# Kernel optimization log

Hardware: AMD Instinct MI355X
Metric: run time of the kernel (lower is better)

## Reference

```python
import jax, jax.numpy as jnp
import numpy as np

N_HEADS = 16
D_HEAD = 64
QUERY_DIM = 1024
CONTEXT_DIM = 1024
INNER = N_HEADS * D_HEAD


def setup_inputs() -> dict:
    key = jax.random.key(0)
    ks = jax.random.split(key, 7)
    B, Nq, Nk = 4, 1024, 1024
    x = jax.random.normal(ks[0], (B, Nq, QUERY_DIM), dtype=jnp.float32)
    context = jax.random.normal(ks[1], (B, Nk, CONTEXT_DIM), dtype=jnp.float32)
    s_q = 1.0 / np.sqrt(QUERY_DIM)
    s_c = 1.0 / np.sqrt(CONTEXT_DIM)
    s_i = 1.0 / np.sqrt(INNER)
    Wq = jax.random.uniform(ks[2], (QUERY_DIM, INNER), jnp.float32, -s_q, s_q)
    Wk = jax.random.uniform(ks[3], (CONTEXT_DIM, INNER), jnp.float32, -s_c, s_c)
    Wv = jax.random.uniform(ks[4], (CONTEXT_DIM, INNER), jnp.float32, -s_c, s_c)
    Wo = jax.random.uniform(ks[5], (INNER, QUERY_DIM), jnp.float32, -s_i, s_i)
    bo = jax.random.uniform(ks[6], (QUERY_DIM,), jnp.float32, -s_i, s_i)
    return {"x": x, "context": context, "Wq": Wq, "Wk": Wk, "Wv": Wv, "Wo": Wo, "bo": bo}


def reference(x, context, Wq, Wk, Wv, Wo, bo):
    B, Nq, _ = x.shape
    Nk = context.shape[1]
    scale = D_HEAD ** -0.5
    # project and split heads: [B, H, N, d]
    q = (x @ Wq).reshape(B, Nq, N_HEADS, D_HEAD).transpose(0, 2, 1, 3)
    k = (context @ Wk).reshape(B, Nk, N_HEADS, D_HEAD).transpose(0, 2, 1, 3)
    v = (context @ Wv).reshape(B, Nk, N_HEADS, D_HEAD).transpose(0, 2, 1, 3)
    scores = jnp.einsum("bhqd,bhkd->bhqk", q, k) * scale
    attn = jax.nn.softmax(scores, axis=-1)
    out = jnp.einsum("bhqk,bhkd->bhqd", attn, v)
    out = out.transpose(0, 2, 1, 3).reshape(B, Nq, INNER)
    return out @ Wo + bo
```

## Files before the change

### kernel.cpp

```cpp
#include <hip/hip_runtime.h>
#include <hip/hip_bf16.h>

#define BATCH 4
#define NQ 1024
#define NKK 1024
#define HD 1024
#define NHEADS 16

typedef __bf16 bf16x8 __attribute__((ext_vector_type(8)));
typedef float f32x4 __attribute__((ext_vector_type(4)));
typedef unsigned short u16;
typedef unsigned int u32;

__device__ __forceinline__ u16 f2bf(float f) {
    union { float f; u32 u; } v; v.f = f;
    u32 r = v.u + 0x7FFFu + ((v.u >> 16) & 1u);
    return (u16)(r >> 16);
}

#define GLOAD16(gp, lp) \
    __builtin_amdgcn_global_load_lds((const __attribute__((address_space(1))) void*)(gp), \
                                     (__attribute__((address_space(3))) void*)(lp), 16, 0, 0)

#define MFMA16(a, b, c) __builtin_amdgcn_mfma_f32_16x16x32_bf16(a, b, c, 0, 0, 0)

__global__ __launch_bounds__(256) void cvt2bf_k(const float* __restrict__ a,
                                                u16* __restrict__ o, int n4) {
    int i = blockIdx.x * blockDim.x + threadIdx.x;
    const int stride = gridDim.x * blockDim.x;
    for (; i < n4; i += stride) {
        float4 v = ((const float4*)a)[i];
        ushort4 p;
        p.x = f2bf(v.x); p.y = f2bf(v.y); p.z = f2bf(v.z); p.w = f2bf(v.w);
        ((ushort4*)o)[i] = p;
    }
}

__global__ __launch_bounds__(256) void transpose4_k(const float* __restrict__ w0,
                                                    const float* __restrict__ w1,
                                                    const float* __restrict__ w2,
                                                    const float* __restrict__ w3,
                                                    u16* __restrict__ ws) {
    const float* src = blockIdx.z == 0 ? w0 : blockIdx.z == 1 ? w1 : blockIdx.z == 2 ? w2 : w3;
    const float scl = (blockIdx.z == 0) ? 0.18033688011112042f : 1.0f;
    u16* dst = ws + (size_t)blockIdx.z * (1024u * 1024u);
    __shared__ u16 t[64][65];
    const int bx = blockIdx.x * 64;
    const int by = blockIdx.y * 64;
    const int tid = threadIdx.x;
#pragma unroll
    for (int p = 0; p < 16; ++p) {
        int idx = p * 256 + tid;
        int r = idx >> 6, c = idx & 63;
        t[c][r] = f2bf(scl * src[(size_t)(by + r) * 1024 + bx + c]);
    }
    __syncthreads();
#pragma unroll
    for (int p = 0; p < 16; ++p) {
        int idx = p * 256 + tid;
        int r = idx >> 6, c = idx & 63;
        dst[(size_t)(bx + r) * 1024 + by + c] = t[r][c];
    }
}

__global__ __launch_bounds__(256) void gemm_qkv(const u16* __restrict__ Xb,
                                                const u16* __restrict__ Cb,
                                                const u16* __restrict__ WqT,
                                                const u16* __restrict__ WkT,
                                                const u16* __restrict__ WvT,
                                                u16* __restrict__ Qb,
                                                u16* __restrict__ Kb,
                                                u16* __restrict__ VTb) {
    const int bid = blockIdx.x;
    const int swz = (bid & 7) * 192 + (bid >> 3);
    const int z = swz / 512;
    const int rem = swz - z * 512;
    const int m0 = (rem >> 3) * 64;
    const int n0 = (rem & 7) * 128;

    const u16* __restrict__ A  = (z == 0) ? Xb : Cb;
    const u16* __restrict__ BT = (z == 0) ? WqT : (z == 1) ? WkT : WvT;

    __shared__ __align__(16) u16 Asm[64 * 32];
    __shared__ __align__(16) u16 Bsm[128 * 32];

    const int tid = threadIdx.x, lane = tid & 63, wv = tid >> 6;
    const int wm = wv >> 1, wn = wv & 1;
    const int lr = lane & 15, lg = lane >> 4;
    const int M = BATCH * NQ, N = HD, K = HD;

    const int sa = wv * 64 + lane;
    const int ra = sa >> 2, ka = (sa & 3) * 8;
    const int cb0 = (wv * 2) * 64, cb1 = (wv * 2 + 1) * 64;
    const int s0 = cb0 + lane, s1 = cb1 + lane;
    const int r0 = s0 >> 2, k0 = (s0 & 3) * 8;
    const int r1 = s1 >> 2, k1 = (s1 & 3) * 8;

    f32x4 acc[2][4];
#pragma unroll
    for (int i = 0; i < 2; ++i)
#pragma unroll
        for (int j = 0; j < 4; ++j) acc[i][j] = (f32x4)(0.0f);

    for (int kt = 0; kt < K; kt += 32) {
        __syncthreads();
        GLOAD16(A + (size_t)(m0 + ra) * K + kt + ka, &Asm[(wv * 64) * 8]);
        GLOAD16(BT + (size_t)(n0 + r0) * K + kt + k0, &Bsm[cb0 * 8]);
        GLOAD16(BT + (size_t)(n0 + r1) * K + kt + k1, &Bsm[cb1 * 8]);
        __syncthreads();
        bf16x8 af[2], bfr[4];
#pragma unroll
        for (int m = 0; m < 2; ++m)
            af[m] = *(const bf16x8*)&Asm[(wm * 32 + m * 16 + lr) * 32 + lg * 8];
#pragma unroll
        for (int n = 0; n < 4; ++n)
            bfr[n] = *(const bf16x8*)&Bsm[(wn * 64 + n * 16 + lr) * 32 + lg * 8];
#pragma unroll
        for (int m = 0; m < 2; ++m)
#pragma unroll
            for (int n = 0; n < 4; ++n)
                acc[m][n] = MFMA16(af[m], bfr[n], acc[m][n]);
    }

    if (z < 2) {
        u16* __restrict__ C = (z == 0) ? Qb : Kb;
#pragma unroll
        for (int m = 0; m < 2; ++m)
#pragma unroll
            for (int n = 0; n < 4; ++n) {
                const int col = n0 + wn * 64 + n * 16 + lr;
                const int rb = m0 + wm * 32 + m * 16 + lg * 4;
#pragma unroll
                for (int r = 0; r < 4; ++r)
                    C[(size_t)(rb + r) * N + col] = f2bf(acc[m][n][r]);
            }
    } else {
#pragma unroll
        for (int m = 0; m < 2; ++m)
#pragma unroll
            for (int n = 0; n < 4; ++n) {
                const int col = n0 + wn * 64 + n * 16 + lr;
                const int rb = m0 + wm * 32 + m * 16 + lg * 4;
                ushort4 pk;
                pk.x = f2bf(acc[m][n][0]);
                pk.y = f2bf(acc[m][n][1]);
                pk.z = f2bf(acc[m][n][2]);
                pk.w = f2bf(acc[m][n][3]);
                *(ushort4*)&VTb[(size_t)col * M + rb] = pk;
            }
    }
}

__global__ __launch_bounds__(256) void gemm_out(const u16* __restrict__ A,
                                                const u16* __restrict__ BT,
                                                const float* __restrict__ bias,
                                                float* __restrict__ C) {
    const int bid = blockIdx.x;
    const int swz = (bid & 7) * 64 + (bid >> 3);
    const int m0 = (swz >> 3) * 64;
    const int n0 = (swz & 7) * 128;

    __shared__ __align__(16) u16 Asm[64 * 32];
    __shared__ __align__(16) u16 Bsm[128 * 32];

    const int tid = threadIdx.x, lane = tid & 63, wv = tid >> 6;
    const int wm = wv >> 1, wn = wv & 1;
    const int lr = lane & 15, lg = lane >> 4;
    const int N = HD, K = HD;

    const int sa = wv * 64 + lane;
    const int ra = sa >> 2, ka = (sa & 3) * 8;
    const int cb0 = (wv * 2) * 64, cb1 = (wv * 2 + 1) * 64;
    const int s0 = cb0 + lane, s1 = cb1 + lane;
    const int r0 = s0 >> 2, k0 = (s0 & 3) * 8;
    const int r1 = s1 >> 2, k1 = (s1 & 3) * 8;

    f32x4 acc[2][4];
#pragma unroll
    for (int i = 0; i < 2; ++i)
#pragma unroll
        for (int j = 0; j < 4; ++j) acc[i][j] = (f32x4)(0.0f);

    for (int kt = 0; kt < K; kt += 32) {
        __syncthreads();
        GLOAD16(A + (size_t)(m0 + ra) * K + kt + ka, &Asm[(wv * 64) * 8]);
        GLOAD16(BT + (size_t)(n0 + r0) * K + kt + k0, &Bsm[cb0 * 8]);
        GLOAD16(BT + (size_t)(n0 + r1) * K + kt + k1, &Bsm[cb1 * 8]);
        __syncthreads();
        bf16x8 af[2], bfr[4];
#pragma unroll
        for (int m = 0; m < 2; ++m)
            af[m] = *(const bf16x8*)&Asm[(wm * 32 + m * 16 + lr) * 32 + lg * 8];
#pragma unroll
        for (int n = 0; n < 4; ++n)
            bfr[n] = *(const bf16x8*)&Bsm[(wn * 64 + n * 16 + lr) * 32 + lg * 8];
#pragma unroll
        for (int m = 0; m < 2; ++m)
#pragma unroll
            for (int n = 0; n < 4; ++n)
                acc[m][n] = MFMA16(af[m], bfr[n], acc[m][n]);
    }

#pragma unroll
    for (int m = 0; m < 2; ++m)
#pragma unroll
        for (int n = 0; n < 4; ++n) {
            const int col = n0 + wn * 64 + n * 16 + lr;
            const int rb = m0 + wm * 32 + m * 16 + lg * 4;
            const float bv = bias[col];
#pragma unroll
            for (int r = 0; r < 4; ++r)
                C[(size_t)(rb + r) * N + col] = acc[m][n][r] + bv;
        }
}

__global__ __launch_bounds__(256) void attn_k(const u16* __restrict__ Q,
                                              const u16* __restrict__ Kp,
                                              const u16* __restrict__ VT,
                                              u16* __restrict__ AO) {
    __shared__ __align__(16) u16 Ksm[2][64 * 64];
    __shared__ __align__(16) u16 Vsm[2][64 * 64];
    __shared__ __align__(16) u16 Psm[4][16 * 64];

    const int tid = threadIdx.x, lane = tid & 63, wv = tid >> 6;
    const int lr = lane & 15, lg = lane >> 4;

    const int swz = (blockIdx.x & 7) * 128 + (blockIdx.x >> 3);
    const int bh = swz >> 4;
    const int b = bh >> 4, h = bh & 15;
    const int q0 = (swz & 15) * 64 + wv * 16;
    const int lx = lr & 7;

    bf16x8 qf[2];
#pragma unroll
    for (int ks = 0; ks < 2; ++ks)
        qf[ks] = *(const bf16x8*)&Q[(size_t)(b * NQ + q0 + lr) * HD +
                                    h * 64 + ks * 32 + lg * 8];

    const int kbase = b * NKK, vrow0 = h * 64;
    auto stageKV = [&](int kt, int bufsel) {
#pragma unroll
        for (int i = 0; i < 2; ++i) {
            const int cb = (wv * 2 + i) * 64;
            const int s = cb + lane;
            const int row = s >> 3;
            const int cg = (s & 7) ^ (row & 7);
            GLOAD16(Kp + (size_t)(kbase + kt + row) * HD + h * 64 + cg * 8,
                    &Ksm[bufsel][cb * 8]);
            GLOAD16(VT + (size_t)(vrow0 + row) * (BATCH * NKK) + kbase + kt + cg * 8,
                    &Vsm[bufsel][cb * 8]);
        }
    };

    float sum[4] = {0.0f, 0.0f, 0.0f, 0.0f};
    f32x4 o[4];
#pragma unroll
    for (int n = 0; n < 4; ++n) o[n] = (f32x4)(0.0f);

    stageKV(0, 0);
    __syncthreads();
    int cur = 0;

    for (int t = 0; t < NKK / 64; ++t) {
        if (t + 1 < NKK / 64) stageKV((t + 1) * 64, cur ^ 1);
        const u16* Ks = &Ksm[cur][0];
        const u16* Vs = &Vsm[cur][0];

        f32x4 s[4];
#pragma unroll
        for (int n = 0; n < 4; ++n) s[n] = (f32x4)(0.0f);
#pragma unroll
        for (int n = 0; n < 4; ++n) {
            bf16x8 kf0 = *(const bf16x8*)&Ks[(n * 16 + lr) * 64 + (lg ^ lx) * 8];
            bf16x8 kf1 = *(const bf16x8*)&Ks[(n * 16 + lr) * 64 + ((lg | 4) ^ lx) * 8];
            s[n] = MFMA16(qf[0], kf0, s[n]);
            s[n] = MFMA16(qf[1], kf1, s[n]);
        }

        u16* P = &Psm[wv][0];
#pragma unroll
        for (int n = 0; n < 4; ++n)
#pragma unroll
            for (int r = 0; r < 4; ++r) {
                const float p = exp2f(s[n][r]);
                sum[r] += p;
                const int row = lg * 4 + r;
                const int c = n * 2 + (lr >> 3);
                P[row * 64 + ((c ^ (row & 7)) * 8) + (lr & 7)] = f2bf(p);
            }

#pragma unroll
        for (int ks = 0; ks < 2; ++ks) {
            bf16x8 pa = *(const bf16x8*)&P[lr * 64 + (((ks * 4 + lg) ^ lx)) * 8];
#pragma unroll
            for (int n = 0; n < 4; ++n) {
                bf16x8 vf = *(const bf16x8*)&Vs[(n * 16 + lr) * 64 + (((ks * 4 + lg) ^ lx)) * 8];
                o[n] = MFMA16(pa, vf, o[n]);
            }
        }
        __syncthreads();
        cur ^= 1;
    }

    float rs[4];
#pragma unroll
    for (int r = 0; r < 4; ++r) {
        float v = sum[r];
#pragma unroll
        for (int d = 1; d < 16; d <<= 1) v += __shfl_xor(v, d);
        rs[r] = 1.0f / v;
    }

#pragma unroll
    for (int n = 0; n < 4; ++n)
#pragma unroll
        for (int r = 0; r < 4; ++r) {
            const float v = o[n][r] * rs[r];
            AO[(size_t)(b * NQ + q0 + lg * 4 + r) * HD +
               h * 64 + n * 16 + lr] = f2bf(v);
        }
}

extern "C" void kernel_launch(void* const* d_in, const int* in_sizes, int n_in,
                              void* d_out, int out_size, void* d_ws, size_t ws_size,
                              hipStream_t stream) {
    const float* x   = (const float*)d_in[0];
    const float* ctx = (const float*)d_in[1];
    const float* Wq  = (const float*)d_in[2];
    const float* Wk  = (const float*)d_in[3];
    const float* Wv  = (const float*)d_in[4];
    const float* Wo  = (const float*)d_in[5];
    const float* bo  = (const float*)d_in[6];

    u16* ws = (u16*)d_ws;
    const size_t MEG = 1024u * 1024u;
    u16* WqT = ws + 0 * MEG;
    u16* WkT = ws + 1 * MEG;
    u16* WvT = ws + 2 * MEG;
    u16* WoT = ws + 3 * MEG;
    u16* Xb  = ws + 4 * MEG;
    u16* Cb  = ws + 8 * MEG;
    u16* Qb  = ws + 12 * MEG;
    u16* Kb  = ws + 16 * MEG;
    u16* VTb = ws + 20 * MEG;
    u16* AOb = Xb;

    transpose4_k<<<dim3(16, 16, 4), 256, 0, stream>>>(Wq, Wk, Wv, Wo, ws);
    cvt2bf_k<<<4096, 256, 0, stream>>>(x,   Xb, 1024 * 1024);
    cvt2bf_k<<<4096, 256, 0, stream>>>(ctx, Cb, 1024 * 1024);
    gemm_qkv<<<1536, 256, 0, stream>>>(Xb, Cb, WqT, WkT, WvT, Qb, Kb, VTb);
    attn_k<<<1024, 256, 0, stream>>>(Qb, Kb, VTb, AOb);
    gemm_out<<<512, 256, 0, stream>>>(AOb, WoT, bo, (float*)d_out);
}
```

Before: 123.3 us.

## Double GEMM K-tile to 64 with XOR-swizzled LDS layout

The QKV and output projection GEMMs now stage 64-wide K tiles instead of 32, which halves the number of barrier pairs per K loop. The LDS layout XOR-swizzles the 16-byte column groups by row so that fragment reads avoid bank conflicts. The f2bf helper now uses a native __bf16 cast in place of manual bit rounding. This doubles LDS use per block and keeps a single-buffered load-then-compute pattern.

```diff
diff --git a/kernel.cpp b/kernel.cpp
--- a/kernel.cpp
+++ b/kernel.cpp
@@ -13,9 +13,9 @@
 typedef unsigned int u32;
 
 __device__ __forceinline__ u16 f2bf(float f) {
-    union { float f; u32 u; } v; v.f = f;
-    u32 r = v.u + 0x7FFFu + ((v.u >> 16) & 1u);
-    return (u16)(r >> 16);
+    union { __bf16 h; u16 u; } v;
+    v.h = (__bf16)f;
+    return v.u;
 }
 
 #define GLOAD16(gp, lp) \
@@ -81,45 +81,58 @@
     const u16* __restrict__ A  = (z == 0) ? Xb : Cb;
     const u16* __restrict__ BT = (z == 0) ? WqT : (z == 1) ? WkT : WvT;
 
-    __shared__ __align__(16) u16 Asm[64 * 32];
-    __shared__ __align__(16) u16 Bsm[128 * 32];
+    __shared__ __align__(16) u16 Asm[64 * 64];
+    __shared__ __align__(16) u16 Bsm[128 * 64];
 
     const int tid = threadIdx.x, lane = tid & 63, wv = tid >> 6;
     const int wm = wv >> 1, wn = wv & 1;
     const int lr = lane & 15, lg = lane >> 4;
+    const int lx = lr & 7;
     const int M = BATCH * NQ, N = HD, K = HD;
 
-    const int sa = wv * 64 + lane;
-    const int ra = sa >> 2, ka = (sa & 3) * 8;
-    const int cb0 = (wv * 2) * 64, cb1 = (wv * 2 + 1) * 64;
-    const int s0 = cb0 + lane, s1 = cb1 + lane;
-    const int r0 = s0 >> 2, k0 = (s0 & 3) * 8;
-    const int r1 = s1 >> 2, k1 = (s1 & 3) * 8;
-
     f32x4 acc[2][4];
 #pragma unroll
     for (int i = 0; i < 2; ++i)
 #pragma unroll
         for (int j = 0; j < 4; ++j) acc[i][j] = (f32x4)(0.0f);
 
-    for (int kt = 0; kt < K; kt += 32) {
-        __syncthreads();
-        GLOAD16(A + (size_t)(m0 + ra) * K + kt + ka, &Asm[(wv * 64) * 8]);
-        GLOAD16(BT + (size_t)(n0 + r0) * K + kt + k0, &Bsm[cb0 * 8]);
-        GLOAD16(BT + (size_t)(n0 + r1) * K + kt + k1, &Bsm[cb1 * 8]);
-        __syncthreads();
-        bf16x8 af[2], bfr[4];
+    for (int kt = 0; kt < K; kt += 64) {
+        __syncthreads();
+#pragma unroll
+        for (int i = 0; i < 2; ++i) {
+            const int cb = (wv * 2 + i) * 64;
+            const int s = cb + lane;
+            const int row = s >> 3, cg = (s & 7) ^ (row & 7);
+            GLOAD16(A + (size_t)(m0 + row) * K + kt + cg * 8, &Asm[cb * 8]);
+        }
+#pragma unroll
+        for (int i = 0; i < 4; ++i) {
+            const int cb = (wv * 4 + i) * 64;
+            const int s = cb + lane;
+            const int row = s >> 3, cg = (s & 7) ^ (row & 7);
+            GLOAD16(BT + (size_t)(n0 + row) * K + kt + cg * 8, &Bsm[cb * 8]);
+        }
+        __syncthreads();
+        bf16x8 af[2][2], bfr[4][2];
 #pragma unroll
         for (int m = 0; m < 2; ++m)
-            af[m] = *(const bf16x8*)&Asm[(wm * 32 + m * 16 + lr) * 32 + lg * 8];
+#pragma unroll
+            for (int kk = 0; kk < 2; ++kk)
+                af[m][kk] = *(const bf16x8*)&Asm[((wm * 32 + m * 16 + lr) * 8 +
+                                                 ((kk * 4 + lg) ^ lx)) * 8];
 #pragma unroll
         for (int n = 0; n < 4; ++n)
-            bfr[n] = *(const bf16x8*)&Bsm[(wn * 64 + n * 16 + lr) * 32 + lg * 8];
-#pragma unroll
-        for (int m = 0; m < 2; ++m)
-#pragma unroll
-            for (int n = 0; n < 4; ++n)
-                acc[m][n] = MFMA16(af[m], bfr[n], acc[m][n]);
+#pragma unroll
+            for (int kk = 0; kk < 2; ++kk)
+                bfr[n][kk] = *(const bf16x8*)&Bsm[((wn * 64 + n * 16 + lr) * 8 +
+                                                  ((kk * 4 + lg) ^ lx)) * 8];
+#pragma unroll
+        for (int kk = 0; kk < 2; ++kk)
+#pragma unroll
+            for (int m = 0; m < 2; ++m)
+#pragma unroll
+                for (int n = 0; n < 4; ++n)
+                    acc[m][n] = MFMA16(af[m][kk], bfr[n][kk], acc[m][n]);
     }
 
     if (z < 2) {
@@ -160,45 +173,58 @@
     const int m0 = (swz >> 3) * 64;
     const int n0 = (swz & 7) * 128;
 
-    __shared__ __align__(16) u16 Asm[64 * 32];
-    __shared__ __align__(16) u16 Bsm[128 * 32];
+    __shared__ __align__(16) u16 Asm[64 * 64];
+    __shared__ __align__(16) u16 Bsm[128 * 64];
 
     const int tid = threadIdx.x, lane = tid & 63, wv = tid >> 6;
     const int wm = wv >> 1, wn = wv & 1;
     const int lr = lane & 15, lg = lane >> 4;
+    const int lx = lr & 7;
     const int N = HD, K = HD;
 
-    const int sa = wv * 64 + lane;
-    const int ra = sa >> 2, ka = (sa & 3) * 8;
-    const int cb0 = (wv * 2) * 64, cb1 = (wv * 2 + 1) * 64;
-    const int s0 = cb0 + lane, s1 = cb1 + lane;
-    const int r0 = s0 >> 2, k0 = (s0 & 3) * 8;
-    const int r1 = s1 >> 2, k1 = (s1 & 3) * 8;
-
     f32x4 acc[2][4];
 #pragma unroll
     for (int i = 0; i < 2; ++i)
 #pragma unroll
         for (int j = 0; j < 4; ++j) acc[i][j] = (f32x4)(0.0f);
 
-    for (int kt = 0; kt < K; kt += 32) {
-        __syncthreads();
-        GLOAD16(A + (size_t)(m0 + ra) * K + kt + ka, &Asm[(wv * 64) * 8]);
-        GLOAD16(BT + (size_t)(n0 + r0) * K + kt + k0, &Bsm[cb0 * 8]);
-        GLOAD16(BT + (size_t)(n0 + r1) * K + kt + k1, &Bsm[cb1 * 8]);
-        __syncthreads();
-        bf16x8 af[2], bfr[4];
+    for (int kt = 0; kt < K; kt += 64) {
+        __syncthreads();
+#pragma unroll
+        for (int i = 0; i < 2; ++i) {
+            const int cb = (wv * 2 + i) * 64;
+            const int s = cb + lane;
+            const int row = s >> 3, cg = (s & 7) ^ (row & 7);
+            GLOAD16(A + (size_t)(m0 + row) * K + kt + cg * 8, &Asm[cb * 8]);
+        }
+#pragma unroll
+        for (int i = 0; i < 4; ++i) {
+            const int cb = (wv * 4 + i) * 64;
+            const int s = cb + lane;
+            const int row = s >> 3, cg = (s & 7) ^ (row & 7);
+            GLOAD16(BT + (size_t)(n0 + row) * K + kt + cg * 8, &Bsm[cb * 8]);
+        }
+        __syncthreads();
+        bf16x8 af[2][2], bfr[4][2];
 #pragma unroll
         for (int m = 0; m < 2; ++m)
-            af[m] = *(const bf16x8*)&Asm[(wm * 32 + m * 16 + lr) * 32 + lg * 8];
+#pragma unroll
+            for (int kk = 0; kk < 2; ++kk)
+                af[m][kk] = *(const bf16x8*)&Asm[((wm * 32 + m * 16 + lr) * 8 +
+                                                 ((kk * 4 + lg) ^ lx)) * 8];
 #pragma unroll
         for (int n = 0; n < 4; ++n)
-            bfr[n] = *(const bf16x8*)&Bsm[(wn * 64 + n * 16 + lr) * 32 + lg * 8];
-#pragma unroll
-        for (int m = 0; m < 2; ++m)
-#pragma unroll
-            for (int n = 0; n < 4; ++n)
-                acc[m][n] = MFMA16(af[m], bfr[n], acc[m][n]);
+#pragma unroll
+            for (int kk = 0; kk < 2; ++kk)
+                bfr[n][kk] = *(const bf16x8*)&Bsm[((wn * 64 + n * 16 + lr) * 8 +
+                                                  ((kk * 4 + lg) ^ lx)) * 8];
+#pragma unroll
+        for (int kk = 0; kk < 2; ++kk)
+#pragma unroll
+            for (int m = 0; m < 2; ++m)
+#pragma unroll
+                for (int n = 0; n < 4; ++n)
+                    acc[m][n] = MFMA16(af[m][kk], bfr[n][kk], acc[m][n]);
     }
 
 #pragma unroll
```

Result: faster. 107.5 us (-12.8%).
